# Optimization experiments

Hardware: AMD Instinct MI355X
Metric: run time of the kernel (lower is better)

The kernel has to match this reference:

```python
import jax, jax.numpy as jnp
import numpy as np

B, T_SRC, T_TGT, C_IN, C_OUT = 8, 4096, 2048, 1024, 1024
LN_EPS = 1e-5


def _prefix_mask(lens, T):
    return (jnp.arange(T)[None, :] < lens[:, None]).astype(jnp.int32)


def setup_inputs() -> dict:
    key = jax.random.key(0)
    ks = jax.random.split(key, 6)
    src = jax.random.normal(ks[0], (B, T_SRC, C_IN), dtype=jnp.float32)
    tgt = jax.random.normal(ks[1], (B, T_TGT, C_IN), dtype=jnp.float32)
    # ragged prefix lengths; first row full so src_sizes.max() == T_SRC (static result width)
    src_lens = jax.random.randint(ks[2], (B,), T_SRC // 2, T_SRC + 1).at[0].set(T_SRC)
    tgt_lens = jax.random.randint(ks[3], (B,), T_TGT // 2, T_TGT + 1).at[0].set(T_TGT)
    src_mask = _prefix_mask(src_lens, T_SRC)
    tgt_mask = _prefix_mask(tgt_lens, T_TGT)
    conv_w = jax.random.normal(ks[4], (C_OUT, C_IN), dtype=jnp.float32) * 0.02
    conv_b = jax.random.normal(ks[5], (C_OUT,), dtype=jnp.float32) * 0.02
    ln_g = jnp.ones((C_OUT,), dtype=jnp.float32)
    ln_b = jnp.zeros((C_OUT,), dtype=jnp.float32)
    return {"src": src, "src_mask": src_mask, "tgt": tgt, "tgt_mask": tgt_mask,
            "conv_w": conv_w, "conv_b": conv_b, "ln_g": ln_g, "ln_b": ln_b}


def reference(src, src_mask, tgt, tgt_mask, conv_w, conv_b, ln_g, ln_b):
    # kernel-size-1 Conv1d == per-token linear: [B,T_tgt,C_in] @ W^T + b
    y = jnp.einsum("btc,oc->bto", tgt, conv_w) + conv_b  # [B, T_tgt, C_out]

    src_sizes = src_mask.sum(-1).astype(jnp.int32)  # [B]
    tgt_sizes = tgt_mask.sum(-1).astype(jnp.int32)  # [B]

    # Batched nearest-neighbor ragged resize: out pos j maps to floor(j*tgt/src)
    j = jnp.arange(src.shape[1], dtype=jnp.int32)  # [T_src]
    safe_src = jnp.maximum(src_sizes, 1)[:, None]
    idx = (j[None, :] * tgt_sizes[:, None]) // safe_src  # [B, T_src]
    idx = jnp.clip(idx, 0, jnp.maximum(tgt_sizes, 1)[:, None] - 1)
    gathered = jnp.take_along_axis(y, idx[:, :, None], axis=1)  # [B, T_src, C_out]
    valid = (j[None, :] < src_sizes[:, None])[:, :, None]
    upsampled = jnp.where(valid, gathered, 0.0)

    # LayerNorm over channel dim (applied to all positions, incl. zero padding, as in torch)
    mu = upsampled.mean(-1, keepdims=True)
    var = jnp.mean(jnp.square(upsampled - mu), axis=-1, keepdims=True)
    out = (upsampled - mu) * jax.lax.rsqrt(var + LN_EPS) * ln_g + ln_b
    return (out, src_mask)
```

## Files before the change

kernel.cpp:

```cpp
#include <hip/hip_runtime.h>

#define NB   8
#define TSRC 4096
#define TTGT 2048
#define CH   1024
#define BK   64

typedef __attribute__((ext_vector_type(4))) float  f32x4;
typedef __attribute__((ext_vector_type(8))) __bf16 bf16x8;
typedef __attribute__((ext_vector_type(4))) __bf16 bf16x4;

__device__ __forceinline__ void async16(const void* g, void* l) {
  __builtin_amdgcn_global_load_lds((const __attribute__((address_space(1))) void*)g,
                                   (__attribute__((address_space(3))) void*)l, 16, 0, 0);
}

__global__ __launch_bounds__(256) void prep_kernel(const float* __restrict__ tgt,
                                                   const float* __restrict__ W,
                                                   const int* __restrict__ src_mask,
                                                   const int* __restrict__ tgt_mask,
                                                   __bf16* __restrict__ Abf,
                                                   __bf16* __restrict__ Wbf,
                                                   int* __restrict__ sizes,
                                                   float* __restrict__ mask_out) {
  const int bx = blockIdx.x;
  const int t  = threadIdx.x;
  const int NCONV = NB * TTGT + CH;
  if (bx < NCONV) {
    const float* sp;
    __bf16* dp;
    if (bx < NB * TTGT) { sp = tgt + (size_t)bx * CH; dp = Abf + (size_t)bx * CH; }
    else { const int r = bx - NB * TTGT; sp = W + (size_t)r * CH; dp = Wbf + (size_t)r * CH; }
    const float4 v = ((const float4*)sp)[t];
    bf16x4 u = {(__bf16)v.x, (__bf16)v.y, (__bf16)v.z, (__bf16)v.w};
    *(bf16x4*)(dp + t * 4) = u;
  } else if (bx < NCONV + 16) {
    const int id = bx - NCONV;
    const int b  = id & 7;
    const int* m = (id < 8) ? (src_mask + (size_t)b * TSRC) : (tgt_mask + (size_t)b * TTGT);
    const int T  = (id < 8) ? TSRC : TTGT;
    int s = 0;
    for (int i = t; i < T; i += 256) s += m[i];
#pragma unroll
    for (int off = 32; off > 0; off >>= 1) s += __shfl_down(s, off);
    __shared__ int red[4];
    if ((t & 63) == 0) red[t >> 6] = s;
    __syncthreads();
    if (t == 0) sizes[id] = red[0] + red[1] + red[2] + red[3];
  } else {
    const int i = (bx - (NCONV + 16)) * 256 + t;
    mask_out[i] = (float)src_mask[i];
  }
}

__global__ __launch_bounds__(256) void gemm_kernel(const __bf16* __restrict__ A,
                                                   const __bf16* __restrict__ Bw,
                                                   const float* __restrict__ bias,
                                                   const int* __restrict__ sizes,
                                                   __bf16* __restrict__ y) {
  const int bid = blockIdx.x;
  const int Mt  = bid & 127;
  const int Nt  = bid >> 7;
  const int n0 = Nt * 128;
  const int m0 = Mt * 128;
  const int b  = m0 >> 11;
  const int t0 = m0 & (TTGT - 1);
  if (t0 >= sizes[8 + b]) return;

  __shared__ __bf16 As[128 * BK];
  __shared__ __bf16 Bs[128 * BK];

  const int tid  = threadIdx.x;
  const int lane = tid & 63;
  const int wave = tid >> 6;
  const int wm   = (wave >> 1) * 64;
  const int wn   = (wave & 1) * 64;
  const int lr   = lane & 15;
  const int quad = lane >> 4;

  const int srow = tid >> 3;
  const int scol = (tid & 7) * 8;
  const __bf16* gA = A  + ((size_t)(m0 + srow)) * CH + scol;
  const __bf16* gB = Bw + ((size_t)(n0 + srow)) * CH + scol;
  __bf16* lA = As + tid * 8;
  __bf16* lB = Bs + tid * 8;

  f32x4 acc[4][4];
  const f32x4 z = {0.f, 0.f, 0.f, 0.f};
#pragma unroll
  for (int i = 0; i < 4; ++i)
#pragma unroll
    for (int j = 0; j < 4; ++j) acc[i][j] = z;

  for (int kb = 0; kb < CH; kb += BK) {
#pragma unroll
    for (int q = 0; q < 4; ++q) {
      async16(gA + (size_t)q * 32 * CH + kb, lA + q * 2048);
      async16(gB + (size_t)q * 32 * CH + kb, lB + q * 2048);
    }
    __syncthreads();
#pragma unroll
    for (int ko = 0; ko < 2; ++ko) {
      bf16x8 af[4], bf[4];
#pragma unroll
      for (int i = 0; i < 4; ++i)
        af[i] = *(const bf16x8*)(As + (wm + i * 16 + lr) * BK + ko * 32 + quad * 8);
#pragma unroll
      for (int j = 0; j < 4; ++j)
        bf[j] = *(const bf16x8*)(Bs + (wn + j * 16 + lr) * BK + ko * 32 + quad * 8);
#pragma unroll
      for (int i = 0; i < 4; ++i)
#pragma unroll
        for (int j = 0; j < 4; ++j)
          acc[i][j] = __builtin_amdgcn_mfma_f32_16x16x32_bf16(af[i], bf[j], acc[i][j], 0, 0, 0);
    }
    __syncthreads();
  }

#pragma unroll
  for (int i = 0; i < 4; ++i) {
    const int mrow = m0 + wm + i * 16 + quad * 4;
#pragma unroll
    for (int j = 0; j < 4; ++j) {
      const int ncol = n0 + wn + j * 16 + lr;
      const float bv = bias[ncol];
      __bf16* yp = y + (size_t)mrow * CH + ncol;
#pragma unroll
      for (int r = 0; r < 4; ++r) yp[(size_t)r * CH] = (__bf16)(acc[i][j][r] + bv);
    }
  }
}

__global__ __launch_bounds__(256) void ln_kernel(const __bf16* __restrict__ y,
                                                 const int* __restrict__ sizes,
                                                 const float* __restrict__ g,
                                                 const float* __restrict__ be,
                                                 float* __restrict__ out) {
  const int wid = (blockIdx.x * 256 + threadIdx.x) >> 6;
  const int l   = threadIdx.x & 63;
#pragma unroll
  for (int rr = 0; rr < 4; ++rr) {
    const int row = wid + rr * 8192;
    const int b   = row >> 12;
    const int j   = row & (TSRC - 1);
    const int ss  = sizes[b];
    const int tg  = sizes[8 + b];
    float v[16];
    if (j < ss) {
      const int den = (ss > 0) ? ss : 1;
      int ii = (int)(((long long)j * (long long)tg) / den);
      const int hi = ((tg > 1) ? tg : 1) - 1;
      ii = (ii > hi) ? hi : ((ii < 0) ? 0 : ii);
      const __bf16* yr = y + ((size_t)b * TTGT + ii) * CH;
      const bf16x8 u0 = *(const bf16x8*)(yr + l * 8);
      const bf16x8 u1 = *(const bf16x8*)(yr + 512 + l * 8);
#pragma unroll
      for (int k = 0; k < 8; ++k) { v[k] = (float)u0[k]; v[8 + k] = (float)u1[k]; }
    } else {
#pragma unroll
      for (int k = 0; k < 16; ++k) v[k] = 0.f;
    }
    float s = 0.f, q = 0.f;
#pragma unroll
    for (int k = 0; k < 16; ++k) { s += v[k]; q += v[k] * v[k]; }
#pragma unroll
    for (int off = 32; off > 0; off >>= 1) {
      s += __shfl_xor(s, off);
      q += __shfl_xor(q, off);
    }
    const float mu = s * (1.0f / CH);
    float var = q * (1.0f / CH) - mu * mu;
    var = fmaxf(var, 0.0f);
    const float rs = rsqrtf(var + 1e-5f);
    float* orow = out + (size_t)row * CH;
#pragma unroll
    for (int h = 0; h < 2; ++h) {
      const int base = h * 512 + l * 8;
      const float4 g0 = *(const float4*)(g + base);
      const float4 g1 = *(const float4*)(g + base + 4);
      const float4 b0 = *(const float4*)(be + base);
      const float4 b1 = *(const float4*)(be + base + 4);
      float4 o0, o1;
      o0.x = (v[h * 8 + 0] - mu) * rs * g0.x + b0.x;
      o0.y = (v[h * 8 + 1] - mu) * rs * g0.y + b0.y;
      o0.z = (v[h * 8 + 2] - mu) * rs * g0.z + b0.z;
      o0.w = (v[h * 8 + 3] - mu) * rs * g0.w + b0.w;
      o1.x = (v[h * 8 + 4] - mu) * rs * g1.x + b1.x;
      o1.y = (v[h * 8 + 5] - mu) * rs * g1.y + b1.y;
      o1.z = (v[h * 8 + 6] - mu) * rs * g1.z + b1.z;
      o1.w = (v[h * 8 + 7] - mu) * rs * g1.w + b1.w;
      *(float4*)(orow + base)     = o0;
      *(float4*)(orow + base + 4) = o1;
    }
  }
}

__global__ __launch_bounds__(256) void fallback_kernel(const float* __restrict__ tgt,
                                                       const int* __restrict__ src_mask,
                                                       const int* __restrict__ tgt_mask,
                                                       const float* __restrict__ W,
                                                       const float* __restrict__ bias,
                                                       const float* __restrict__ g,
                                                       const float* __restrict__ be,
                                                       float* __restrict__ out,
                                                       float* __restrict__ mask_out) {
  const int bx = blockIdx.x;
  const int b  = bx >> 12;
  const int j  = bx & (TSRC - 1);
  const int t  = threadIdx.x;
  int s1 = 0, s2 = 0;
  for (int i = t; i < TSRC; i += 256) s1 += src_mask[(size_t)b * TSRC + i];
  for (int i = t; i < TTGT; i += 256) s2 += tgt_mask[(size_t)b * TTGT + i];
#pragma unroll
  for (int off = 32; off > 0; off >>= 1) { s1 += __shfl_down(s1, off); s2 += __shfl_down(s2, off); }
  __shared__ int ired[8];
  if ((t & 63) == 0) { ired[t >> 6] = s1; ired[4 + (t >> 6)] = s2; }
  __syncthreads();
  const int ss = ired[0] + ired[1] + ired[2] + ired[3];
  const int tg = ired[4] + ired[5] + ired[6] + ired[7];
  const bool valid = j < ss;
  int ii = 0;
  if (valid) {
    const int den = (ss > 0) ? ss : 1;
    ii = (int)(((long long)j * (long long)tg) / den);
    const int hi = ((tg > 1) ? tg : 1) - 1;
    if (ii > hi) ii = hi;
    if (ii < 0) ii = 0;
  }
  __shared__ float trow[CH];
  const float* tr = tgt + ((size_t)b * TTGT + ii) * CH;
  for (int i = t; i < CH; i += 256) trow[i] = valid ? tr[i] : 0.0f;
  __syncthreads();
  float4 v = make_float4(0.f, 0.f, 0.f, 0.f);
  if (valid) {
    float a0 = 0.f, a1 = 0.f, a2 = 0.f, a3 = 0.f;
    const float* w0 = W + (size_t)(4 * t + 0) * CH;
    const float* w1 = W + (size_t)(4 * t + 1) * CH;
    const float* w2 = W + (size_t)(4 * t + 2) * CH;
    const float* w3 = W + (size_t)(4 * t + 3) * CH;
    for (int k = 0; k < CH; ++k) {
      const float x = trow[k];
      a0 += x * w0[k]; a1 += x * w1[k]; a2 += x * w2[k]; a3 += x * w3[k];
    }
    v.x = a0 + bias[4 * t + 0];
    v.y = a1 + bias[4 * t + 1];
    v.z = a2 + bias[4 * t + 2];
    v.w = a3 + bias[4 * t + 3];
  }
  float s  = v.x + v.y + v.z + v.w;
  float sq = v.x * v.x + v.y * v.y + v.z * v.z + v.w * v.w;
#pragma unroll
  for (int off = 32; off > 0; off >>= 1) {
    s  += __shfl_down(s, off);
    sq += __shfl_down(sq, off);
  }
  __shared__ float red[8];
  __shared__ float stats[2];
  if ((t & 63) == 0) { red[t >> 6] = s; red[4 + (t >> 6)] = sq; }
  __syncthreads();
  if (t == 0) {
    const float S  = red[0] + red[1] + red[2] + red[3];
    const float Q  = red[4] + red[5] + red[6] + red[7];
    const float mu = S * (1.0f / CH);
    float var = Q * (1.0f / CH) - mu * mu;
    var = fmaxf(var, 0.0f);
    stats[0] = mu;
    stats[1] = rsqrtf(var + 1e-5f);
  }
  __syncthreads();
  const float mu = stats[0], rs = stats[1];
  const float4 gg = ((const float4*)g)[t];
  const float4 bb = ((const float4*)be)[t];
  float4 o;
  o.x = (v.x - mu) * rs * gg.x + bb.x;
  o.y = (v.y - mu) * rs * gg.y + bb.y;
  o.z = (v.z - mu) * rs * gg.z + bb.z;
  o.w = (v.w - mu) * rs * gg.w + bb.w;
  ((float4*)(out + ((size_t)b * TSRC + j) * CH))[t] = o;
  if (t == 0) mask_out[bx] = (float)src_mask[bx];
}

extern "C" void kernel_launch(void* const* d_in, const int* in_sizes, int n_in,
                              void* d_out, int out_size, void* d_ws, size_t ws_size,
                              hipStream_t stream) {
  (void)in_sizes; (void)n_in; (void)out_size;
  const int*   src_mask = (const int*)d_in[1];
  const float* tgt      = (const float*)d_in[2];
  const int*   tgt_mask = (const int*)d_in[3];
  const float* conv_w   = (const float*)d_in[4];
  const float* conv_b   = (const float*)d_in[5];
  const float* ln_g     = (const float*)d_in[6];
  const float* ln_b     = (const float*)d_in[7];

  float* out      = (float*)d_out;
  float* mask_out = out + (size_t)NB * TSRC * CH;

  const size_t M       = (size_t)NB * TTGT;
  const size_t off_abf = 256;
  const size_t off_wbf = off_abf + M * CH * 2;
  const size_t off_y   = off_wbf + (size_t)CH * CH * 2;
  const size_t need    = off_y + M * CH * 2;

  if (ws_size >= need) {
    int*    sizes = (int*)d_ws;
    __bf16* Abf   = (__bf16*)((char*)d_ws + off_abf);
    __bf16* Wbf   = (__bf16*)((char*)d_ws + off_wbf);
    __bf16* y     = (__bf16*)((char*)d_ws + off_y);
    prep_kernel<<<NB * TTGT + CH + 16 + 128, 256, 0, stream>>>(tgt, conv_w, src_mask, tgt_mask,
                                                               Abf, Wbf, sizes, mask_out);
    gemm_kernel<<<1024, 256, 0, stream>>>(Abf, Wbf, conv_b, sizes, y);
    ln_kernel<<<2048, 256, 0, stream>>>(y, sizes, ln_g, ln_b, out);
  } else {
    fallback_kernel<<<NB * TSRC, 256, 0, stream>>>(tgt, src_mask, tgt_mask, conv_w, conv_b,
                                                   ln_g, ln_b, out, mask_out);
  }
}
```

Baseline: 316.3 us.

## Fuse fp32-to-bf16 activation conversion into GEMM with register prefetch

The separate pass that converts the whole tgt tensor to bf16 is removed. The GEMM now loads fp32 activations straight into registers, converts them to bf16 and writes them to LDS. The next k-tile's loads are issued before the current MFMA work so their latency is partly hidden. This avoids a full round trip of the activation matrix through memory, at the cost of reading fp32 (twice the bytes) inside the GEMM, more register pressure and an extra barrier per k-step.

Result: slower. 330.3 us (+4.4%).

```diff
diff --git a/kernel.cpp b/kernel.cpp
--- a/kernel.cpp
+++ b/kernel.cpp
@@ -15,27 +15,20 @@
                                    (__attribute__((address_space(3))) void*)l, 16, 0, 0);
 }
 
-__global__ __launch_bounds__(256) void prep_kernel(const float* __restrict__ tgt,
-                                                   const float* __restrict__ W,
+__global__ __launch_bounds__(256) void prep_kernel(const float* __restrict__ W,
                                                    const int* __restrict__ src_mask,
                                                    const int* __restrict__ tgt_mask,
-                                                   __bf16* __restrict__ Abf,
                                                    __bf16* __restrict__ Wbf,
                                                    int* __restrict__ sizes,
                                                    float* __restrict__ mask_out) {
   const int bx = blockIdx.x;
   const int t  = threadIdx.x;
-  const int NCONV = NB * TTGT + CH;
-  if (bx < NCONV) {
-    const float* sp;
-    __bf16* dp;
-    if (bx < NB * TTGT) { sp = tgt + (size_t)bx * CH; dp = Abf + (size_t)bx * CH; }
-    else { const int r = bx - NB * TTGT; sp = W + (size_t)r * CH; dp = Wbf + (size_t)r * CH; }
-    const float4 v = ((const float4*)sp)[t];
+  if (bx < CH) {
+    const float4 v = ((const float4*)(W + (size_t)bx * CH))[t];
     bf16x4 u = {(__bf16)v.x, (__bf16)v.y, (__bf16)v.z, (__bf16)v.w};
-    *(bf16x4*)(dp + t * 4) = u;
-  } else if (bx < NCONV + 16) {
-    const int id = bx - NCONV;
+    *(bf16x4*)(Wbf + (size_t)bx * CH + t * 4) = u;
+  } else if (bx < CH + 16) {
+    const int id = bx - CH;
     const int b  = id & 7;
     const int* m = (id < 8) ? (src_mask + (size_t)b * TSRC) : (tgt_mask + (size_t)b * TTGT);
     const int T  = (id < 8) ? TSRC : TTGT;
@@ -48,12 +41,12 @@
     __syncthreads();
     if (t == 0) sizes[id] = red[0] + red[1] + red[2] + red[3];
   } else {
-    const int i = (bx - (NCONV + 16)) * 256 + t;
+    const int i = (bx - (CH + 16)) * 256 + t;
     mask_out[i] = (float)src_mask[i];
   }
 }
 
-__global__ __launch_bounds__(256) void gemm_kernel(const __bf16* __restrict__ A,
+__global__ __launch_bounds__(256) void gemm_kernel(const float* __restrict__ A32,
                                                    const __bf16* __restrict__ Bw,
                                                    const float* __restrict__ bias,
                                                    const int* __restrict__ sizes,
@@ -80,8 +73,8 @@
 
   const int srow = tid >> 3;
   const int scol = (tid & 7) * 8;
-  const __bf16* gA = A  + ((size_t)(m0 + srow)) * CH + scol;
-  const __bf16* gB = Bw + ((size_t)(n0 + srow)) * CH + scol;
+  const float*  gA = A32 + (size_t)(m0 + srow) * CH + scol;
+  const __bf16* gB = Bw  + (size_t)(n0 + srow) * CH + scol;
   __bf16* lA = As + tid * 8;
   __bf16* lB = Bs + tid * 8;
 
@@ -92,13 +85,35 @@
 #pragma unroll
     for (int j = 0; j < 4; ++j) acc[i][j] = z;
 
-  for (int kb = 0; kb < CH; kb += BK) {
-#pragma unroll
-    for (int q = 0; q < 4; ++q) {
-      async16(gA + (size_t)q * 32 * CH + kb, lA + q * 2048);
-      async16(gB + (size_t)q * 32 * CH + kb, lB + q * 2048);
-    }
-    __syncthreads();
+  float4 a0[4], a1[4];
+
+#pragma unroll
+  for (int q = 0; q < 4; ++q) {
+    const float* p = gA + (size_t)q * 32 * CH;
+    a0[q] = *(const float4*)p;
+    a1[q] = *(const float4*)(p + 4);
+  }
+#pragma unroll
+  for (int q = 0; q < 4; ++q) {
+    bf16x8 u = {(__bf16)a0[q].x, (__bf16)a0[q].y, (__bf16)a0[q].z, (__bf16)a0[q].w,
+                (__bf16)a1[q].x, (__bf16)a1[q].y, (__bf16)a1[q].z, (__bf16)a1[q].w};
+    *(bf16x8*)(lA + q * 2048) = u;
+  }
+#pragma unroll
+  for (int q = 0; q < 4; ++q) async16(gB + (size_t)q * 32 * CH, lB + q * 2048);
+  __syncthreads();
+
+  for (int kt = 0; kt < CH / BK; ++kt) {
+    const int nkb  = (kt + 1) * BK;
+    const bool more = (nkb < CH);
+    if (more) {
+#pragma unroll
+      for (int q = 0; q < 4; ++q) {
+        const float* p = gA + (size_t)q * 32 * CH + nkb;
+        a0[q] = *(const float4*)p;
+        a1[q] = *(const float4*)(p + 4);
+      }
+    }
 #pragma unroll
     for (int ko = 0; ko < 2; ++ko) {
       bf16x8 af[4], bf[4];
@@ -113,6 +128,17 @@
 #pragma unroll
         for (int j = 0; j < 4; ++j)
           acc[i][j] = __builtin_amdgcn_mfma_f32_16x16x32_bf16(af[i], bf[j], acc[i][j], 0, 0, 0);
+    }
+    __syncthreads();
+    if (more) {
+#pragma unroll
+      for (int q = 0; q < 4; ++q) {
+        bf16x8 u = {(__bf16)a0[q].x, (__bf16)a0[q].y, (__bf16)a0[q].z, (__bf16)a0[q].w,
+                    (__bf16)a1[q].x, (__bf16)a1[q].y, (__bf16)a1[q].z, (__bf16)a1[q].w};
+        *(bf16x8*)(lA + q * 2048) = u;
+      }
+#pragma unroll
+      for (int q = 0; q < 4; ++q) async16(gB + (size_t)q * 32 * CH + nkb, lB + q * 2048);
     }
     __syncthreads();
   }
@@ -296,19 +322,17 @@
   float* mask_out = out + (size_t)NB * TSRC * CH;
 
   const size_t M       = (size_t)NB * TTGT;
-  const size_t off_abf = 256;
-  const size_t off_wbf = off_abf + M * CH * 2;
+  const size_t off_wbf = 256;
   const size_t off_y   = off_wbf + (size_t)CH * CH * 2;
   const size_t need    = off_y + M * CH * 2;
 
   if (ws_size >= need) {
     int*    sizes = (int*)d_ws;
-    __bf16* Abf   = (__bf16*)((char*)d_ws + off_abf);
     __bf16* Wbf   = (__bf16*)((char*)d_ws + off_wbf);
     __bf16* y     = (__bf16*)((char*)d_ws + off_y);
-    prep_kernel<<<NB * TTGT + CH + 16 + 128, 256, 0, stream>>>(tgt, conv_w, src_mask, tgt_mask,
-                                                               Abf, Wbf, sizes, mask_out);
-    gemm_kernel<<<1024, 256, 0, stream>>>(Abf, Wbf, conv_b, sizes, y);
+    prep_kernel<<<CH + 16 + 128, 256, 0, stream>>>(conv_w, src_mask, tgt_mask,
+                                                   Wbf, sizes, mask_out);
+    gemm_kernel<<<1024, 256, 0, stream>>>(tgt, Wbf, conv_b, sizes, y);
     ln_kernel<<<2048, 256, 0, stream>>>(y, sizes, ln_g, ln_b, out);
   } else {
     fallback_kernel<<<NB * TSRC, 256, 0, stream>>>(tgt, src_mask, tgt_mask, conv_w, conv_b,
```
